# Optimization experiments

Measured on AMD Instinct MI355X. Metric: run time of the kernel, lower is better.

The kernel has to match this reference:

```python
import jax, jax.numpy as jnp
import numpy as np


def _rope(v):
    # v: (B, S, H). Faithful to the torch RotaryEmbedding, including its
    # emb = cat(sin, cos) followed by emb[..., ::2]/[..., 1::2] slicing.
    B, S, H = v.shape
    inv_freq = 1.0 / (10000.0 ** (jnp.arange(0, H, 2, dtype=jnp.float32) / H))  # (H/2,)
    t = jnp.arange(S, dtype=jnp.float32)
    freqs = t[:, None] * inv_freq[None, :]                       # (S, H/2)
    emb = jnp.concatenate([jnp.sin(freqs), jnp.cos(freqs)], -1)  # (S, H)
    x1, x2 = v[..., ::2], v[..., 1::2]                           # (B, S, H/2) each
    emb_sin, emb_cos = emb[..., ::2], emb[..., 1::2]             # (S, H/2) each
    return jnp.concatenate([x1 * emb_cos - x2 * emb_sin,
                            x1 * emb_sin + x2 * emb_cos], -1)


def setup_inputs() -> dict:
    key = jax.random.key(0)
    ks = jax.random.split(key, 9)
    B, S, H = 2, 2048, 512
    sc = 0.02
    return {
        "x": jax.random.normal(ks[0], (B, S, H), dtype=jnp.float32),
        "Wq": jax.random.normal(ks[1], (H, H), dtype=jnp.float32) * sc,
        "bq": jax.random.normal(ks[2], (H,), dtype=jnp.float32) * sc,
        "Wk": jax.random.normal(ks[3], (H, H), dtype=jnp.float32) * sc,
        "bk": jax.random.normal(ks[4], (H,), dtype=jnp.float32) * sc,
        "Wv": jax.random.normal(ks[5], (H, H), dtype=jnp.float32) * sc,
        "bv": jax.random.normal(ks[6], (H,), dtype=jnp.float32) * sc,
        "Wo": jax.random.normal(ks[7], (H, H), dtype=jnp.float32) * sc,
        "bo": jax.random.normal(ks[8], (H,), dtype=jnp.float32) * sc,
    }


WINDOW_SIZE = 128


def reference(x, Wq, bq, Wk, bk, Wv, bv, Wo, bo):
    B, S, H = x.shape
    W = WINDOW_SIZE
    pad = W // 2
    # Projections (torch Linear: x @ W.T + b)
    Q = x @ Wq.T + bq
    K = x @ Wk.T + bk
    V = x @ Wv.T + bv
    rQ = _rope(Q)
    rK = _rope(K)
    # Pad along seq and gather sliding windows: window t covers positions t-pad .. t+pad-1
    pK = jnp.pad(rK, ((0, 0), (pad, pad), (0, 0)))
    pV = jnp.pad(V, ((0, 0), (pad, pad), (0, 0)))
    idx = jnp.arange(S)[:, None] + jnp.arange(W)[None, :]  # (S, W) into padded seq
    Kw = pK[:, idx, :]  # (B, S, W, H)
    Vw = pV[:, idx, :]  # (B, S, W, H)
    scores = jnp.einsum("bth,btwh->btw", rQ, Kw) / jnp.sqrt(jnp.float32(H))
    weights = jax.nn.softmax(scores, axis=-1)
    out = jnp.einsum("btw,btwh->bth", weights, Vw)
    return out @ Wo.T + bo
```

## Files before the change

kernel.cpp:

```cpp
#include <hip/hip_runtime.h>
#include <math.h>

#define S_LEN 2048
#define B_SZ  2
#define H_DIM 512
#define WIN   128
#define PAD   64
#define SP    (S_LEN + WIN)
#define SCALE 0.044194173824159216f
#define TQ    32

typedef __bf16 bf16;
typedef __attribute__((ext_vector_type(8))) __bf16 bf16x8;
typedef __attribute__((ext_vector_type(4))) __bf16 bf16x4;
typedef __attribute__((ext_vector_type(4))) float f32x4;

#define GLDS16(g, l) __builtin_amdgcn_global_load_lds( \
    (const __attribute__((address_space(1))) void*)(g), \
    (__attribute__((address_space(3))) void*)(l), 16, 0, 0)

__global__ __launch_bounds__(256) void prep_k(
    const float* __restrict__ x,
    const float* __restrict__ Wq, const float* __restrict__ Wk,
    const float* __restrict__ Wv, const float* __restrict__ Wo,
    bf16* __restrict__ xb, bf16* __restrict__ wb,
    bf16* __restrict__ pKb, bf16* __restrict__ pVT,
    float* __restrict__ sinT, float* __restrict__ cosT)
{
  int i = blockIdx.x * 256 + threadIdx.x;
  if (i < 262144) {
    int e = i * 8;
    float4 v0 = *(const float4*)(x + e);
    float4 v1 = *(const float4*)(x + e + 4);
    bf16x8 o = {(bf16)v0.x, (bf16)v0.y, (bf16)v0.z, (bf16)v0.w,
                (bf16)v1.x, (bf16)v1.y, (bf16)v1.z, (bf16)v1.w};
    *(bf16x8*)(xb + e) = o;
  } else if (i < 524288) {
    int idx = (i - 262144) * 4;
    int m = idx >> 18;
    const float* src = (m == 0) ? Wq : (m == 1) ? Wk : (m == 2) ? Wv : Wo;
    float4 v = *(const float4*)(src + (idx & 262143));
    bf16x4 hv = {(bf16)v.x, (bf16)v.y, (bf16)v.z, (bf16)v.w};
    *(bf16x4*)(wb + idx) = hv;
  } else if (i < 557056) {
    int idx = i - 524288;
    float4 z = {0.f, 0.f, 0.f, 0.f};
    if (idx < 16384) {
      int b = idx >> 13, r = (idx & 8191) >> 6, c = idx & 63;
      int row = (r < 64) ? r : (S_LEN + r);
      *(float4*)(pKb + ((size_t)b * SP + row) * 512 + c * 8) = z;
    } else {
      int j = idx - 16384;
      int b = j >> 13, h = (j & 8191) >> 4, v = j & 15;
      int col = (v < 8) ? v * 8 : (S_LEN + PAD + (v - 8) * 8);
      *(float4*)(pVT + ((size_t)b * 512 + h) * SP + col) = z;
    }
  } else {
    int idx = i - 557056;
    int s = idx >> 7, jj = idx & 127;
    float fqA = exp2f(-(float)jj * 0.10381025296523f);
    float fqB = exp2f(-(float)(2 * jj + 1) * 0.05190512648262f);
    float aA = (float)s * fqA;
    float aB = (float)s * fqB;
    sinT[s * 256 + jj]       = sinf(aA);
    sinT[s * 256 + jj + 128] = cosf(aA);
    cosT[s * 256 + jj]       = sinf(aB);
    cosT[s * 256 + jj + 128] = cosf(aB);
  }
}

template<int MFR, int MODE>
__global__ __launch_bounds__(256) void gemm_k(
    const bf16* __restrict__ Ab, const bf16* __restrict__ Wb,
    const float* __restrict__ bq, const float* __restrict__ bk,
    const float* __restrict__ bv,
    const float* __restrict__ sinT, const float* __restrict__ cosT,
    bf16* __restrict__ oQ, bf16* __restrict__ oK, bf16* __restrict__ oVT,
    float* __restrict__ oOut)
{
  constexpr int BM = MFR * 32;
  constexpr int ABYTES = BM * 128;
  constexpr int BUFB = ABYTES + 128 * 128;
  __shared__ __align__(16) unsigned char smem[2 * BUFB];
  const int tid = threadIdx.x;
  const int lane = tid & 63, wid = tid >> 6;
  const int wm = wid >> 1, wn = wid & 1;
  const int row0 = blockIdx.x * BM;
  const int wrow0 = (MODE == 0 ? 0 : 1536) + blockIdx.y * 128;
  const int lr = lane & 15, lk = lane >> 4;

  f32x4 acc[MFR][4] = {};

  auto stage = [&](int k0, int bufsel) {
    unsigned char* buf = smem + bufsel * BUFB;
#pragma unroll
    for (int i = 0; i < MFR; i++) {
      int c = tid + i * 256;
      int r = c >> 3, p = c & 7, l = p ^ (r & 7);
      GLDS16(Ab + (size_t)(row0 + r) * 512 + k0 + l * 8, buf + c * 16);
    }
#pragma unroll
    for (int j = 0; j < 4; j++) {
      int c = tid + j * 256;
      int r = c >> 3, p = c & 7, l = p ^ (r & 7);
      GLDS16(Wb + (size_t)(wrow0 + r) * 512 + k0 + l * 8, buf + ABYTES + c * 16);
    }
  };

  stage(0, 0);
  __syncthreads();
  for (int t = 0; t < 8; t++) {
    if (t < 7) stage((t + 1) * 64, (t + 1) & 1);
    const unsigned char* buf = smem + (t & 1) * BUFB;
    bf16x8 bfr[4][2];
#pragma unroll
    for (int ni = 0; ni < 4; ni++) {
      int r = wn * 64 + ni * 16 + lr;
      const unsigned char* base = buf + ABYTES + r * 128;
      int sw = (r & 7) << 4;
      bfr[ni][0] = *(const bf16x8*)(base + ((lk * 16) ^ sw));
      bfr[ni][1] = *(const bf16x8*)(base + ((64 + lk * 16) ^ sw));
    }
#pragma unroll
    for (int mi = 0; mi < MFR; mi++) {
      int r = wm * (MFR * 16) + mi * 16 + lr;
      const unsigned char* base = buf + r * 128;
      int sw = (r & 7) << 4;
      bf16x8 a0 = *(const bf16x8*)(base + ((lk * 16) ^ sw));
      bf16x8 a1 = *(const bf16x8*)(base + ((64 + lk * 16) ^ sw));
#pragma unroll
      for (int ni = 0; ni < 4; ni++) {
        acc[mi][ni] = __builtin_amdgcn_mfma_f32_16x16x32_bf16(a0, bfr[ni][0], acc[mi][ni], 0, 0, 0);
        acc[mi][ni] = __builtin_amdgcn_mfma_f32_16x16x32_bf16(a1, bfr[ni][1], acc[mi][ni], 0, 0, 0);
      }
    }
    __syncthreads();
  }

  const int rowb = row0 + wm * (MFR * 16) + ((lane >> 4) * 4);
  if (MODE == 1) {
#pragma unroll
    for (int mi = 0; mi < MFR; mi++)
#pragma unroll
      for (int ni = 0; ni < 4; ni++) {
        int col = blockIdx.y * 128 + wn * 64 + ni * 16 + (lane & 15);
        float bb = bq[col];
#pragma unroll
        for (int g = 0; g < 4; g++) {
          int rr = rowb + mi * 16 + g;
          oOut[(size_t)rr * 512 + col] = acc[mi][ni][g] + bb;
        }
      }
    return;
  }
  const int region = blockIdx.y >> 2;
  const float* bias = (region == 0) ? bq : (region == 1) ? bk : bv;
  const int cm0 = (blockIdx.y & 3) * 128;
#pragma unroll
  for (int mi = 0; mi < MFR; mi++)
#pragma unroll
    for (int ni = 0; ni < 4; ni++) {
      int c = cm0 + wn * 64 + ni * 16 + (lane & 15);
      float bb = bias[c];
      if (region == 2) {
#pragma unroll
        for (int g = 0; g < 4; g++) {
          int rr = rowb + mi * 16 + g;
          int b = rr >> 11, s = rr & 2047;
          oVT[((size_t)b * 512 + c) * SP + PAD + s] = (bf16)(acc[mi][ni][g] + bb);
        }
      } else {
        int j = c >> 1, par = c & 1;
#pragma unroll
        for (int g = 0; g < 4; g++) {
          int rr = rowb + mi * 16 + g;
          int s = rr & 2047;
          float v = acc[mi][ni][g] + bb;
          float p = __shfl_xor(v, 1);
          float es = sinT[s * 256 + j], ec = cosT[s * 256 + j];
          float res = par ? (p * es + v * ec) : (v * ec - p * es);
          int oc = par ? (j + 256) : j;
          if (region == 0) oQ[(size_t)rr * 512 + oc] = (bf16)res;
          else { int b = rr >> 11; oK[((size_t)b * SP + PAD + s) * 512 + oc] = (bf16)res; }
        }
      }
    }
}

__global__ __launch_bounds__(256) void attn_mfma_k(
    const bf16* __restrict__ rQb, const bf16* __restrict__ pKb,
    const bf16* __restrict__ pVT, bf16* __restrict__ ab)
{
  __shared__ __align__(16) unsigned char smem[53760];
  const int tid = threadIdx.x, lane = tid & 63, w = tid >> 6;
  const int q0g = blockIdx.x * TQ;
  const int nbase = blockIdx.y * 256;
  const int b = q0g >> 11, s0 = q0g & 2047;
  const int lr = lane & 15, lk = lane >> 4;
  const int OFF_K = 4096, OFF_P = 43008;

  f32x4 sacc[5] = {};
  const int tm = w >> 1, tnb = (w & 1) * 5;
  for (int k0 = 0; k0 < 512; k0 += 64) {
    __syncthreads();
    {
      int r = tid >> 3, p = tid & 7, l = p ^ (r & 7);
      GLDS16(rQb + (size_t)(q0g + r) * 512 + k0 + l * 8, smem + (w * 64) * 16);
    }
#pragma unroll
    for (int i = 0; i < 5; i++) {
      int c = tid + i * 256;
      int r = c >> 3, p = c & 7, l = p ^ (r & 7);
      GLDS16(pKb + ((size_t)b * SP + s0 + r) * 512 + k0 + l * 8,
             smem + OFF_K + (i * 256 + w * 64) * 16);
    }
    __syncthreads();
    __builtin_amdgcn_s_setprio(1);
#pragma unroll
    for (int kk = 0; kk < 2; kk++) {
      int arow = tm * 16 + lr;
      bf16x8 a = *(const bf16x8*)(smem + arow * 128 + (((kk * 64 + lk * 16) ^ ((arow & 7) << 4))));
#pragma unroll
      for (int i = 0; i < 5; i++) {
        int brow = (tnb + i) * 16 + lr;
        bf16x8 bb = *(const bf16x8*)(smem + OFF_K + brow * 128 + (((kk * 64 + lk * 16) ^ ((brow & 7) << 4))));
        sacc[i] = __builtin_amdgcn_mfma_f32_16x16x32_bf16(a, bb, sacc[i], 0, 0, 0);
      }
    }
    __builtin_amdgcn_s_setprio(0);
  }
  __syncthreads();
  {
    float* sc = (float*)smem;
#pragma unroll
    for (int i = 0; i < 5; i++) {
      int col = (tnb + i) * 16 + lr;
#pragma unroll
      for (int g = 0; g < 4; g++) {
        int row = tm * 16 + lk * 4 + g;
        sc[row * 164 + col] = sacc[i][g] * SCALE;
      }
    }
  }
  __syncthreads();
  {
    float* sc = (float*)smem;
    bf16* P = (bf16*)(smem + OFF_P);
    int row = tid >> 3, j0 = tid & 7;
    float vals[20];
    float mx = -1e30f;
#pragma unroll
    for (int i = 0; i < 20; i++) {
      int j = j0 + i * 8;
      bool valid = (j >= row) && (j <= row + 127);
      float v = valid ? sc[row * 164 + j] : -1e30f;
      vals[i] = v;
      mx = fmaxf(mx, v);
    }
#pragma unroll
    for (int off = 1; off < 8; off <<= 1) mx = fmaxf(mx, __shfl_xor(mx, off));
    float sum = 0.f;
#pragma unroll
    for (int i = 0; i < 20; i++) {
      float e = (vals[i] > -1e29f) ? __expf(vals[i] - mx) : 0.f;
      vals[i] = e; sum += e;
    }
#pragma unroll
    for (int off = 1; off < 8; off <<= 1) sum += __shfl_xor(sum, off);
    float inv = 1.f / sum;
#pragma unroll
    for (int i = 0; i < 20; i++) {
      int j = j0 + i * 8;
      P[row * 168 + j] = (bf16)(vals[i] * inv);
    }
  }
  const bf16* pVTb = pVT + (size_t)b * 512 * SP;
  const int utm = w >> 1, utnb = (w & 1) * 4;
  for (int n0 = nbase; n0 < nbase + 256; n0 += 128) {
    __syncthreads();
    {
      int r = tid >> 1, half = tid & 1;
      const bf16* src = pVTb + (size_t)(n0 + r) * SP + s0;
#pragma unroll
      for (int i = 0; i < 10; i++) {
        int slot = half * 10 + i;
        float4 v = *(const float4*)(src + slot * 8);
        *(float4*)(smem + r * 336 + slot * 16) = v;
      }
    }
    __syncthreads();
    f32x4 oacc[4] = {};
    __builtin_amdgcn_s_setprio(1);
#pragma unroll
    for (int tk = 0; tk < 5; tk++) {
      int arow = utm * 16 + lr;
      bf16x8 a = *(const bf16x8*)(smem + OFF_P + arow * 336 + tk * 64 + lk * 16);
#pragma unroll
      for (int i = 0; i < 4; i++) {
        int brow = (utnb + i) * 16 + lr;
        bf16x8 bb = *(const bf16x8*)(smem + brow * 336 + tk * 64 + lk * 16);
        oacc[i] = __builtin_amdgcn_mfma_f32_16x16x32_bf16(a, bb, oacc[i], 0, 0, 0);
      }
    }
    __builtin_amdgcn_s_setprio(0);
#pragma unroll
    for (int i = 0; i < 4; i++) {
      int col = n0 + (utnb + i) * 16 + lr;
#pragma unroll
      for (int g = 0; g < 4; g++) {
        int row = utm * 16 + lk * 4 + g;
        ab[(size_t)(q0g + row) * 512 + col] = (bf16)oacc[i][g];
      }
    }
  }
}

extern "C" void kernel_launch(void* const* d_in, const int* in_sizes, int n_in,
                              void* d_out, int out_size, void* d_ws, size_t ws_size,
                              hipStream_t stream) {
  const float* x  = (const float*)d_in[0];
  const float* Wq = (const float*)d_in[1];
  const float* bq = (const float*)d_in[2];
  const float* Wk = (const float*)d_in[3];
  const float* bk = (const float*)d_in[4];
  const float* Wv = (const float*)d_in[5];
  const float* bv = (const float*)d_in[6];
  const float* Wo = (const float*)d_in[7];
  const float* bo = (const float*)d_in[8];
  float* out = (float*)d_out;

  const size_t NQ = (size_t)B_SZ * S_LEN * H_DIM;
  const size_t NP = (size_t)B_SZ * SP * H_DIM;
  float* sinT = (float*)d_ws;
  float* cosT = sinT + (size_t)S_LEN * 256;
  bf16* xb  = (bf16*)(cosT + (size_t)S_LEN * 256);
  bf16* wb  = xb + NQ;
  bf16* rQb = wb + 2048 * 512;
  bf16* pKb = rQb + NQ;
  bf16* pVT = pKb + NP;
  bf16* ab  = pVT + NP;

  prep_k<<<3200, 256, 0, stream>>>(x, Wq, Wk, Wv, Wo, xb, wb,
                                   pKb, pVT, sinT, cosT);

  gemm_k<4, 0><<<dim3(32, 12), 256, 0, stream>>>(xb, wb,
      bq, bk, bv, sinT, cosT, rQb, pKb, pVT, nullptr);

  attn_mfma_k<<<dim3(B_SZ * S_LEN / TQ, 2), 256, 0, stream>>>(rQb, pKb, pVT, ab);

  gemm_k<2, 1><<<dim3(64, 4), 256, 0, stream>>>(ab, wb,
      bo, nullptr, nullptr, sinT, cosT, nullptr, nullptr, nullptr, out);
}
```

Baseline: 48.65 us.

## Double-buffer Q/K and V staging in sliding-window attention kernel

The QK^T loop now prefetches the next 64-wide k-slice of Q and K into a second LDS buffer via global_load_lds while MFMAs run on the current one. The PV stage is reorganised into four 64-column chunks: V is prefetched into registers and written to an alternate LDS buffer after the MFMAs, which hides global latency. The change grows LDS use to about 59.9KB, which may reduce occupancy, and halves MFMA work per sync in the PV stage.

```diff
diff --git a/kernel.cpp b/kernel.cpp
--- a/kernel.cpp
+++ b/kernel.cpp
@@ -191,45 +191,53 @@
     const bf16* __restrict__ rQb, const bf16* __restrict__ pKb,
     const bf16* __restrict__ pVT, bf16* __restrict__ ab)
 {
-  __shared__ __align__(16) unsigned char smem[53760];
+  __shared__ __align__(16) unsigned char smem[59904];
   const int tid = threadIdx.x, lane = tid & 63, w = tid >> 6;
   const int q0g = blockIdx.x * TQ;
   const int nbase = blockIdx.y * 256;
   const int b = q0g >> 11, s0 = q0g & 2047;
   const int lr = lane & 15, lk = lane >> 4;
-  const int OFF_K = 4096, OFF_P = 43008;
+  const int OFF_P = 49152;
 
   f32x4 sacc[5] = {};
   const int tm = w >> 1, tnb = (w & 1) * 5;
-  for (int k0 = 0; k0 < 512; k0 += 64) {
-    __syncthreads();
+
+  auto stageQK = [&](int k0, int sel) {
     {
       int r = tid >> 3, p = tid & 7, l = p ^ (r & 7);
-      GLDS16(rQb + (size_t)(q0g + r) * 512 + k0 + l * 8, smem + (w * 64) * 16);
+      GLDS16(rQb + (size_t)(q0g + r) * 512 + k0 + l * 8,
+             smem + sel * 4096 + tid * 16);
     }
 #pragma unroll
     for (int i = 0; i < 5; i++) {
       int c = tid + i * 256;
       int r = c >> 3, p = c & 7, l = p ^ (r & 7);
       GLDS16(pKb + ((size_t)b * SP + s0 + r) * 512 + k0 + l * 8,
-             smem + OFF_K + (i * 256 + w * 64) * 16);
-    }
-    __syncthreads();
+             smem + 8192 + sel * 20480 + c * 16);
+    }
+  };
+
+  stageQK(0, 0);
+  __syncthreads();
+  for (int t = 0; t < 8; t++) {
+    if (t < 7) stageQK((t + 1) * 64, (t + 1) & 1);
+    const unsigned char* qb = smem + (t & 1) * 4096;
+    const unsigned char* kb = smem + 8192 + (t & 1) * 20480;
     __builtin_amdgcn_s_setprio(1);
 #pragma unroll
     for (int kk = 0; kk < 2; kk++) {
       int arow = tm * 16 + lr;
-      bf16x8 a = *(const bf16x8*)(smem + arow * 128 + (((kk * 64 + lk * 16) ^ ((arow & 7) << 4))));
+      bf16x8 a = *(const bf16x8*)(qb + arow * 128 + (((kk * 64 + lk * 16) ^ ((arow & 7) << 4))));
 #pragma unroll
       for (int i = 0; i < 5; i++) {
         int brow = (tnb + i) * 16 + lr;
-        bf16x8 bb = *(const bf16x8*)(smem + OFF_K + brow * 128 + (((kk * 64 + lk * 16) ^ ((brow & 7) << 4))));
+        bf16x8 bb = *(const bf16x8*)(kb + brow * 128 + (((kk * 64 + lk * 16) ^ ((brow & 7) << 4))));
         sacc[i] = __builtin_amdgcn_mfma_f32_16x16x32_bf16(a, bb, sacc[i], 0, 0, 0);
       }
     }
     __builtin_amdgcn_s_setprio(0);
-  }
-  __syncthreads();
+    __syncthreads();
+  }
   {
     float* sc = (float*)smem;
 #pragma unroll
@@ -275,43 +283,55 @@
     }
   }
   const bf16* pVTb = pVT + (size_t)b * 512 * SP;
-  const int utm = w >> 1, utnb = (w & 1) * 4;
-  for (int n0 = nbase; n0 < nbase + 256; n0 += 128) {
-    __syncthreads();
-    {
-      int r = tid >> 1, half = tid & 1;
-      const bf16* src = pVTb + (size_t)(n0 + r) * SP + s0;
-#pragma unroll
-      for (int i = 0; i < 10; i++) {
-        int slot = half * 10 + i;
-        float4 v = *(const float4*)(src + slot * 8);
-        *(float4*)(smem + r * 336 + slot * 16) = v;
-      }
-    }
-    __syncthreads();
-    f32x4 oacc[4] = {};
+  const int vr = tid >> 2, vq = tid & 3;
+  float4 vreg[5];
+  auto loadV = [&](int n0) {
+    const bf16* src = pVTb + (size_t)(n0 + vr) * SP + s0;
+#pragma unroll
+    for (int i = 0; i < 5; i++)
+      vreg[i] = *(const float4*)(src + (vq * 5 + i) * 8);
+  };
+  auto writeV = [&](int sel) {
+    unsigned char* dst = smem + sel * 21504 + vr * 336;
+#pragma unroll
+    for (int i = 0; i < 5; i++)
+      *(float4*)(dst + (vq * 5 + i) * 16) = vreg[i];
+  };
+
+  loadV(nbase);
+  __syncthreads();
+  writeV(0);
+  __syncthreads();
+  const int cp = w & 1;
+  const int utm = w >> 1;
+  for (int c = 0; c < 4; c++) {
+    int n0 = nbase + c * 64;
+    if (c < 3) loadV(n0 + 64);
+    const unsigned char* vb = smem + (c & 1) * 21504;
+    f32x4 oacc[2] = {};
     __builtin_amdgcn_s_setprio(1);
 #pragma unroll
     for (int tk = 0; tk < 5; tk++) {
-      int arow = utm * 16 + lr;
-      bf16x8 a = *(const bf16x8*)(smem + OFF_P + arow * 336 + tk * 64 + lk * 16);
-#pragma unroll
-      for (int i = 0; i < 4; i++) {
-        int brow = (utnb + i) * 16 + lr;
-        bf16x8 bb = *(const bf16x8*)(smem + brow * 336 + tk * 64 + lk * 16);
+      bf16x8 a = *(const bf16x8*)(smem + OFF_P + (utm * 16 + lr) * 336 + tk * 64 + lk * 16);
+#pragma unroll
+      for (int i = 0; i < 2; i++) {
+        int brow = cp * 32 + i * 16 + lr;
+        bf16x8 bb = *(const bf16x8*)(vb + brow * 336 + tk * 64 + lk * 16);
         oacc[i] = __builtin_amdgcn_mfma_f32_16x16x32_bf16(a, bb, oacc[i], 0, 0, 0);
       }
     }
     __builtin_amdgcn_s_setprio(0);
-#pragma unroll
-    for (int i = 0; i < 4; i++) {
-      int col = n0 + (utnb + i) * 16 + lr;
+    if (c < 3) writeV((c + 1) & 1);
+#pragma unroll
+    for (int i = 0; i < 2; i++) {
+      int col = n0 + (cp * 2 + i) * 16 + lr;
 #pragma unroll
       for (int g = 0; g < 4; g++) {
         int row = utm * 16 + lk * 4 + g;
         ab[(size_t)(q0g + row) * 512 + col] = (bf16)oacc[i][g];
       }
     }
+    __syncthreads();
   }
 }
 
```

New measurement: 71.62 us. 47.2% more time.
